# Kernel tuning notes

Hardware: AMD Instinct MI355X
Metric: run time of the kernel (lower is better)

Reference implementation:

```python
import jax, jax.numpy as jnp
import numpy as np

N_NODES, N_EDGES, N_REL, F_DIM, N_HEAD, N_LAYERS = 20000, 100000, 1000, 128, 4, 4
NEG_SLOPE = 0.2  # PyG GATv2Conv default negative_slope


def _gatv2_layer(x, ea_full, src, dst, Wl, bl, Wr, br, We, att, bias):
    # x: [N, F]; ea_full: [Etot, F] edge attrs (incl. self-loop rows)
    N = x.shape[0]
    H, C = att.shape  # heads, out-dim per head
    xl = (x @ Wl + bl).reshape(N, H, C)          # source-side projection
    xr = (x @ Wr + br).reshape(N, H, C)          # target-side projection
    ee = (ea_full @ We).reshape(-1, H, C)        # [Etot, H, C] edge embedding
    # GATv2 scoring: leaky_relu(x_i + x_j + e) . att
    e = jax.nn.leaky_relu(xl[src] + xr[dst] + ee, NEG_SLOPE)
    logits = jnp.einsum('ehc,hc->eh', e, att)    # [Etot, H]
    # segment softmax over edges grouped by destination node
    m = jax.ops.segment_max(logits, dst, num_segments=N)
    p = jnp.exp(logits - m[dst])
    denom = jax.ops.segment_sum(p, dst, num_segments=N)
    alpha = p / denom[dst]                       # [Etot, H]
    out = jax.ops.segment_sum(alpha[:, :, None] * xl[src], dst, num_segments=N)
    return out.mean(axis=1) + bias               # concat=False -> head mean


def setup_inputs() -> dict:
    key = jax.random.key(0)
    ks = jax.random.split(key, 12)
    N, E, R, F, H, L = N_NODES, N_EDGES, N_REL, F_DIM, N_HEAD, N_LAYERS
    HC = H * F
    s = 1.0 / np.sqrt(F)
    return {
        'x': jax.random.normal(ks[0], (N, F), jnp.float32),
        'edge_index': jax.random.randint(ks[1], (2, E), 0, N, dtype=jnp.int32),
        'relations': jax.random.normal(ks[2], (R, F), jnp.float32),
        'relation_index': jax.random.randint(ks[3], (E,), 0, R, dtype=jnp.int32),
        'Wl': jax.random.normal(ks[4], (L, F, HC), jnp.float32) * s,
        'bl': jnp.zeros((L, HC), jnp.float32),
        'Wr': jax.random.normal(ks[5], (L, F, HC), jnp.float32) * s,
        'br': jnp.zeros((L, HC), jnp.float32),
        'We': jax.random.normal(ks[6], (L, F, HC), jnp.float32) * s,
        'att': jax.random.normal(ks[7], (L, H, F), jnp.float32) * s,
        'bias': jnp.zeros((L, F), jnp.float32),
    }


def reference(x, edge_index, relations, relation_index, Wl, bl, Wr, br, We, att, bias):
    N = x.shape[0]
    sl = jnp.arange(N, dtype=edge_index.dtype)
    src = jnp.concatenate([edge_index[0], sl])   # add_self_loops=True
    dst = jnp.concatenate([edge_index[1], sl])
    ea = relations[relation_index]               # [E, F]
    # self-loop edge_attr uses fill_value='mean' (PyG default)
    ea_mean = ea.mean(axis=0)
    ea_full = jnp.concatenate([ea, jnp.broadcast_to(ea_mean, (N, ea.shape[1]))])
    h = x
    for l in range(N_LAYERS):
        h = _gatv2_layer(h, ea_full, src, dst, Wl[l], bl[l], Wr[l], br[l], We[l], att[l], bias[l])
    return (h, relations)
```

## Files before the change

kernel.cpp:

```cpp
#include <hip/hip_runtime.h>
#include <hip/hip_bf16.h>

#define N_NODES   20000
#define N_EDGES   100000
#define N_REL     1000
#define F_DIM     128
#define N_HEAD    4
#define HC        512
#define HC2       256
#define N_LAYERS  4
#define REL_EXT_ROWS 1008
#define NEG_SLOPE 0.2f
#define NODE_MB   ((N_NODES + 63) / 64)
#define REL_MB    ((REL_EXT_ROWS + 63) / 64)

typedef __attribute__((ext_vector_type(8))) short short8;
typedef __attribute__((ext_vector_type(4))) float floatx4;

__device__ __forceinline__ float loadIn(const void* p, size_t i, int f32) {
    if (f32) return ((const float*)p)[i];
    union { unsigned int u; float f; } c;
    c.u = ((unsigned int)((const unsigned short*)p)[i]) << 16;
    return c.f;
}

__device__ __forceinline__ unsigned short f2bf(float v) {
    __hip_bfloat16 b = __float2bfloat16(v);
    return *(unsigned short*)&b;
}

__device__ __forceinline__ void unpack2(unsigned int u, float& lo, float& hi) {
    union { unsigned int u; float f; } a, b;
    a.u = u << 16;
    b.u = u & 0xFFFF0000u;
    lo = a.f; hi = b.f;
}

__global__ void detect_kernel(const unsigned short* __restrict__ x, int* __restrict__ flag) {
    int t = threadIdx.x;
    int cnt = 0;
    for (int j = t; j < 256; j += 64) {
        int e = (x[j] >> 7) & 0xFF;
        if (e >= 143) cnt++;
    }
    for (int off = 32; off; off >>= 1) cnt += __shfl_xor(cnt, off);
    if (t == 0) flag[0] = (cnt >= 8) ? 1 : 0;
}


__global__ void hist_kernel(const int* __restrict__ dst, const int* __restrict__ rel,
                            int* __restrict__ deg, int* __restrict__ rcount) {
    int e = blockIdx.x * 256 + threadIdx.x;
    if (e < N_EDGES) {
        atomicAdd(&deg[dst[e]], 1);
        atomicAdd(&rcount[rel[e]], 1);
    }
}

__global__ void ea_mean_kernel(const int* __restrict__ rcount,
                               const void* __restrict__ relations,
                               float* __restrict__ ea_mean, const int* __restrict__ flag) {
    int f32 = flag[0];
    int b = blockIdx.x;
    int t = threadIdx.x;
    int col = t & 127;
    int rhalf = t >> 7;
    float acc = 0.f;
    for (int j = 0; j < 4; ++j) {
        int r = b * 8 + j * 2 + rhalf;
        acc += (float)rcount[r] * loadIn(relations, (size_t)r * F_DIM + col, f32);
    }
    __shared__ float part[256];
    part[t] = acc;
    __syncthreads();
    if (t < 128)
        atomicAdd(&ea_mean[col], (part[t] + part[t + 128]) * (1.f / (float)N_EDGES));
}

__global__ void relext_kernel(const void* __restrict__ relations,
                              const float* __restrict__ ea_mean,
                              unsigned short* __restrict__ rel_ext, const int* __restrict__ flag) {
    int idx = blockIdx.x * 256 + threadIdx.x;
    if (idx >= REL_EXT_ROWS * F_DIM) return;
    int f32 = flag[0];
    int r = idx >> 7;
    int c = idx & 127;
    float v;
    if (r < N_REL)       v = loadIn(relations, idx, f32);
    else if (r == N_REL) v = ea_mean[c];
    else                 v = 0.f;
    rel_ext[idx] = f2bf(v);
}

__global__ void scan_kernel(const int* __restrict__ deg,
                            int* __restrict__ row_start, int* __restrict__ cursor) {
    __shared__ int part[1024];
    int t = threadIdx.x;
    const int CH = (N_NODES + 1023) / 1024;
    int base = t * CH;
    int sum = 0;
    for (int j = 0; j < CH; ++j) {
        int idx = base + j;
        if (idx < N_NODES) sum += deg[idx];
    }
    part[t] = sum;
    __syncthreads();
    for (int off = 1; off < 1024; off <<= 1) {
        int u = (t >= off) ? part[t - off] : 0;
        __syncthreads();
        part[t] += u;
        __syncthreads();
    }
    int run = part[t] - sum;
    for (int j = 0; j < CH; ++j) {
        int idx = base + j;
        if (idx < N_NODES) {
            row_start[idx] = run;
            cursor[idx] = run;
            run += deg[idx];
        }
    }
    if (t == 1023) row_start[N_NODES] = part[1023];
}

__global__ void scatter_kernel(const int* __restrict__ src, const int* __restrict__ dst,
                               const int* __restrict__ rel, int* __restrict__ cursor,
                               int* __restrict__ csr_pack) {
    int e = blockIdx.x * 256 + threadIdx.x;
    if (e < N_EDGES) {
        int d = dst[e];
        int p = atomicAdd(&cursor[d], 1);
        csr_pack[p] = src[e] | (rel[e] << 16);
    }
}

__global__ void tail_kernel(const void* __restrict__ relations, void* __restrict__ out,
                            const int* __restrict__ flag) {
    int i = blockIdx.x * 256 + threadIdx.x;
    if (i >= N_REL * F_DIM) return;
    int f32 = flag[0];
    float v = loadIn(relations, i, f32);
    size_t o = (size_t)N_NODES * F_DIM + i;
    if (f32) ((float*)out)[o] = v;
    else     ((unsigned short*)out)[o] = f2bf(v);
}

__global__ void w_transpose_kernel(const void* __restrict__ Wl, const void* __restrict__ Wr,
                                   const void* __restrict__ We,
                                   unsigned short* __restrict__ Wt, const int* __restrict__ flag) {
    int f32 = flag[0];
    int k0 = blockIdx.x * 64;
    int n0 = blockIdx.y * 64;
    int mat = blockIdx.z;
    const void* src = (mat < 4) ? Wl : (mat < 8 ? Wr : We);
    size_t base = (size_t)(mat & 3) * F_DIM * HC;
    unsigned short* dst = Wt + (size_t)mat * HC * F_DIM;
    __shared__ float T[64][65];
    int t = threadIdx.x;
    int r = t >> 2, cq = t & 3;
    for (int j = 0; j < 16; ++j) {
        int n = cq * 16 + j;
        T[n][r] = loadIn(src, base + (size_t)(k0 + r) * HC + n0 + n, f32);
    }
    __syncthreads();
    for (int j = 0; j < 16; ++j) {
        int k = cq * 16 + j;
        dst[(size_t)(n0 + r) * F_DIM + k0 + k] = f2bf(T[r][k]);
    }
}

__launch_bounds__(256, 4)
__global__ void proj_kernel(const void* __restrict__ A_node, int a_input,
                            const unsigned short* __restrict__ rel_ext,
                            const unsigned short* __restrict__ Wlt,
                            const unsigned short* __restrict__ Wrt,
                            const unsigned short* __restrict__ Wet,
                            const void* __restrict__ bl, const void* __restrict__ br,
                            size_t boff,
                            unsigned short* __restrict__ xl,
                            unsigned short* __restrict__ xr,
                            unsigned short* __restrict__ re,
                            const int* __restrict__ flag) {
    __shared__ __align__(16) short As[64][136];
    __shared__ __align__(16) short BtRaw[128 * 72];
    int f32 = flag[0];
    int isNode = (blockIdx.x < NODE_MB);
    int m0 = (isNode ? blockIdx.x : (blockIdx.x - NODE_MB)) * 64;
    int M = isNode ? N_NODES : REL_EXT_ROWS;
    int tpb = isNode ? 2 : 1;
    int a_f32 = (isNode && a_input) ? f32 : 0;
    const void* A = isNode ? A_node : (const void*)rel_ext;
    int t = threadIdx.x;

    for (int j = 0; j < 4; ++j) {
        int c = t + j * 256;
        int row = c >> 4;
        int colc = (c & 15) * 8;
        int gm = m0 + row;
        short8 v = (short8){0, 0, 0, 0, 0, 0, 0, 0};
        if (gm < M) {
            size_t idx = (size_t)gm * F_DIM + colc;
            if (a_f32) {
                const float* Af = (const float*)A;
                for (int q = 0; q < 8; ++q) v[q] = (short)f2bf(Af[idx + q]);
            } else {
                v = *(const short8*)((const unsigned short*)A + idx);
            }
        }
        *(short8*)&As[row][colc] = v;
    }

    int wave = t >> 6, lane = t & 63;
    int wm = (wave >> 1) * 32, wn = (wave & 1) * 64;
    int r16 = lane & 15, quad = lane >> 4;

    for (int it = 0; it < tpb; ++it) {
        int nt = isNode ? (blockIdx.y * 2 + it) : blockIdx.y;
        const unsigned short* Wt = isNode ? ((nt < 4) ? Wlt : Wrt) : Wet;
        int n0 = (nt & 3) * 128;

        floatx4 acc[2][4];
        for (int mi = 0; mi < 2; ++mi)
            for (int ni = 0; ni < 4; ++ni)
                acc[mi][ni] = (floatx4){0.f, 0.f, 0.f, 0.f};

        for (int half = 0; half < 2; ++half) {
            __syncthreads();
            for (int j = 0; j < 4; ++j) {
                int c = t + j * 256;
                int nl = c >> 3;
                int kc = (c & 7) * 8;
                *(short8*)&BtRaw[nl * 72 + kc] =
                    *(const short8*)(Wt + (size_t)(n0 + nl) * F_DIM + half * 64 + kc);
            }
            __syncthreads();

            for (int kk = 0; kk < 2; ++kk) {
                short8 a[2], b[4];
                for (int mi = 0; mi < 2; ++mi)
                    a[mi] = *(const short8*)&As[wm + mi * 16 + r16][half * 64 + kk * 32 + quad * 8];
                for (int ni = 0; ni < 4; ++ni)
                    b[ni] = *(const short8*)&BtRaw[(wn + ni * 16 + r16) * 72 + kk * 32 + quad * 8];
                for (int mi = 0; mi < 2; ++mi)
                    for (int ni = 0; ni < 4; ++ni)
                        acc[mi][ni] = __builtin_amdgcn_mfma_f32_16x16x32_bf16(a[mi], b[ni], acc[mi][ni], 0, 0, 0);
            }
        }

        const void* bias = isNode ? ((nt < 4) ? bl : br) : nullptr;
        unsigned short* out = isNode ? ((nt < 4) ? xl : xr) : re;
        __syncthreads();
        for (int mi = 0; mi < 2; ++mi) {
            for (int ni = 0; ni < 4; ++ni) {
                int col = wn + ni * 16 + r16;
                float bv = bias ? loadIn(bias, boff + n0 + col, f32) : 0.f;
                for (int r = 0; r < 4; ++r) {
                    int rowl = wm + mi * 16 + quad * 4 + r;
                    BtRaw[rowl * 136 + col] = (short)f2bf(acc[mi][ni][r] + bv);
                }
            }
        }
        __syncthreads();
        for (int j = 0; j < 4; ++j) {
            int c = t + j * 256;
            int rowl = c >> 4;
            int colc = (c & 15) * 8;
            int gm = m0 + rowl;
            if (gm < M)
                *(short8*)(out + (size_t)gm * HC + n0 + colc) =
                    *(const short8*)&BtRaw[rowl * 136 + colc];
        }
    }
}

__launch_bounds__(256)
__global__ void edge_kernel(const unsigned int* __restrict__ xl2,
                            const unsigned int* __restrict__ xr2,
                            const unsigned int* __restrict__ re2,
                            const int* __restrict__ row_start,
                            const int* __restrict__ csr_pack,
                            const void* __restrict__ att, size_t att_off,
                            const void* __restrict__ bias, size_t bias_off,
                            void* __restrict__ hout, int final_layer,
                            const int* __restrict__ flag) {
    int f32 = flag[0];
    int i = blockIdx.x;
    int h = threadIdx.x >> 6;
    int lane = threadIdx.x & 63;
    int pidx = h * 64 + lane;

    float xr0, xr1; unpack2(xr2[(size_t)i * HC2 + pidx], xr0, xr1);
    float a0 = loadIn(att, att_off + h * F_DIM + 2 * lane, f32);
    float a1 = loadIn(att, att_off + h * F_DIM + 2 * lane + 1, f32);
    float er0, er1; unpack2(re2[(size_t)N_REL * HC2 + pidx], er0, er1);

    float xs0, xs1; unpack2(xl2[(size_t)i * HC2 + pidx], xs0, xs1);
    float t0 = xs0 + xr0 + er0;
    float t1 = xs1 + xr1 + er1;
    t0 = fmaxf(t0, NEG_SLOPE * t0);
    t1 = fmaxf(t1, NEG_SLOPE * t1);
    float part = t0 * a0 + t1 * a1;
    for (int off = 32; off; off >>= 1) part += __shfl_xor(part, off);
    part = fminf(fmaxf(part, -60.f), 60.f);
    float p = __expf(part);
    float s = p, acc0 = p * xs0, acc1 = p * xs1;

    int e0 = row_start[i], e1 = row_start[i + 1];
    if (e0 < 0) e0 = 0;
    if (e1 > N_EDGES) e1 = N_EDGES;
    if (e1 < e0) e1 = e0;

    unsigned int xv[4], rv[4];
    #pragma unroll
    for (int k = 0; k < 4; ++k) { xv[k] = 0; rv[k] = 0; }
    int b = e0;
    int nb = e1 - b; if (nb > 4) nb = 4;
    #pragma unroll
    for (int k = 0; k < 4; ++k) {
        if (k < nb) {
            int pk = csr_pack[b + k];
            int sn = pk & 0xFFFF;        if (sn >= N_NODES) sn = 0;
            int rn = (pk >> 16) & 0x3FF; if (rn > N_REL) rn = N_REL;
            xv[k] = xl2[(size_t)sn * HC2 + pidx];
            rv[k] = re2[(size_t)rn * HC2 + pidx];
        }
    }
    while (b < e1) {
        int bn = b + 4;
        int nbn = e1 - bn; if (nbn > 4) nbn = 4; if (nbn < 0) nbn = 0;
        unsigned int xvn[4], rvn[4];
        #pragma unroll
        for (int k = 0; k < 4; ++k) { xvn[k] = 0; rvn[k] = 0; }
        #pragma unroll
        for (int k = 0; k < 4; ++k) {
            if (k < nbn) {
                int pk = csr_pack[bn + k];
                int sn = pk & 0xFFFF;        if (sn >= N_NODES) sn = 0;
                int rn = (pk >> 16) & 0x3FF; if (rn > N_REL) rn = N_REL;
                xvn[k] = xl2[(size_t)sn * HC2 + pidx];
                rvn[k] = re2[(size_t)rn * HC2 + pidx];
            }
        }
        #pragma unroll
        for (int k = 0; k < 4; ++k) {
            if (k < nb) {
                float xl0, xl1; unpack2(xv[k], xl0, xl1);
                float ee0, ee1; unpack2(rv[k], ee0, ee1);
                float u0 = xl0 + xr0 + ee0;
                float u1 = xl1 + xr1 + ee1;
                u0 = fmaxf(u0, NEG_SLOPE * u0);
                u1 = fmaxf(u1, NEG_SLOPE * u1);
                float pe = u0 * a0 + u1 * a1;
                for (int off = 32; off; off >>= 1) pe += __shfl_xor(pe, off);
                pe = fminf(fmaxf(pe, -60.f), 60.f);
                float pp = __expf(pe);
                s += pp;
                acc0 += pp * xl0;
                acc1 += pp * xl1;
            }
        }
        #pragma unroll
        for (int k = 0; k < 4; ++k) { xv[k] = xvn[k]; rv[k] = rvn[k]; }
        b = bn; nb = nbn;
    }

    float inv = 1.f / s;
    __shared__ float lsum[N_HEAD][F_DIM];
    lsum[h][2 * lane]     = acc0 * inv;
    lsum[h][2 * lane + 1] = acc1 * inv;
    __syncthreads();
    if (threadIdx.x < F_DIM) {
        int c = threadIdx.x;
        float v = (lsum[0][c] + lsum[1][c] + lsum[2][c] + lsum[3][c]) * 0.25f
                + loadIn(bias, bias_off + c, f32);
        size_t o = (size_t)i * F_DIM + c;
        if (final_layer && f32) ((float*)hout)[o] = v;
        else                    ((unsigned short*)hout)[o] = f2bf(v);
    }
}


extern "C" void kernel_launch(void* const* d_in, const int* in_sizes, int n_in,
                              void* d_out, int out_size, void* d_ws, size_t ws_size,
                              hipStream_t stream) {
    const void* x          = d_in[0];
    const int*  edge_index = (const int*)d_in[1];
    const void* relations  = d_in[2];
    const int*  rel_index  = (const int*)d_in[3];
    const void* Wl         = d_in[4];
    const void* bl         = d_in[5];
    const void* Wr         = d_in[6];
    const void* br         = d_in[7];
    const void* We         = d_in[8];
    const void* att        = d_in[9];
    const void* bias       = d_in[10];

    char* ws = (char*)d_ws;
    size_t off = 0;
    auto alloc = [&](size_t bytes) -> void* {
        void* p = ws + off;
        off = (off + bytes + 255) & ~(size_t)255;
        return p;
    };
    int*            flag     = (int*)alloc(4);
    char*           zero0    = ws + off;
    int*            deg      = (int*)alloc(N_NODES * 4);
    int*            rcount   = (int*)alloc(N_REL * 4);
    float*          ea_mean  = (float*)alloc(F_DIM * 4);
    size_t          zlen     = (size_t)((ws + off) - zero0);
    int*            row_start= (int*)alloc((N_NODES + 1) * 4);
    int*            cursor   = (int*)alloc(N_NODES * 4);
    int*            csr_pack = (int*)alloc(N_EDGES * 4);
    unsigned short* rel_ext  = (unsigned short*)alloc((size_t)REL_EXT_ROWS * F_DIM * 2);
    unsigned short* Wt       = (unsigned short*)alloc((size_t)12 * HC * F_DIM * 2);
    unsigned short* re       = (unsigned short*)alloc((size_t)REL_EXT_ROWS * HC * 2);
    unsigned short* hbuf     = (unsigned short*)alloc((size_t)N_NODES * F_DIM * 2);
    unsigned short* xl       = (unsigned short*)alloc((size_t)N_NODES * HC * 2);
    unsigned short* xr       = (unsigned short*)alloc((size_t)N_NODES * HC * 2);

    const int* esrc = edge_index;
    const int* edst = edge_index + N_EDGES;

    detect_kernel<<<1, 64, 0, stream>>>((const unsigned short*)x, flag);
    hipMemsetAsync(zero0, 0, zlen, stream);
    hist_kernel<<<(N_EDGES + 255) / 256, 256, 0, stream>>>(edst, rel_index, deg, rcount);
    ea_mean_kernel<<<N_REL / 8, 256, 0, stream>>>(rcount, relations, ea_mean, flag);
    relext_kernel<<<(REL_EXT_ROWS * F_DIM + 255) / 256, 256, 0, stream>>>(relations, ea_mean, rel_ext, flag);
    scan_kernel<<<1, 1024, 0, stream>>>(deg, row_start, cursor);
    scatter_kernel<<<(N_EDGES + 255) / 256, 256, 0, stream>>>(esrc, edst, rel_index, cursor, csr_pack);
    w_transpose_kernel<<<dim3(2, 8, 12), 256, 0, stream>>>(Wl, Wr, We, Wt, flag);
    tail_kernel<<<(N_REL * F_DIM + 255) / 256, 256, 0, stream>>>(relations, d_out, flag);

    const void* hin = x;
    int a_input = 1;
    for (int l = 0; l < N_LAYERS; ++l) {
        const unsigned short* Wlt = Wt + (size_t)l * HC * F_DIM;
        const unsigned short* Wrt = Wt + (size_t)(4 + l) * HC * F_DIM;
        const unsigned short* Wet = Wt + (size_t)(8 + l) * HC * F_DIM;
        proj_kernel<<<dim3(NODE_MB + REL_MB, 4), 256, 0, stream>>>(
            hin, a_input, rel_ext, Wlt, Wrt, Wet,
            bl, br, (size_t)l * HC,
            xl, xr, re, flag);
        int final_layer = (l == N_LAYERS - 1);
        void* hout = final_layer ? d_out : (void*)hbuf;
        edge_kernel<<<N_NODES, 256, 0, stream>>>(
            (const unsigned int*)xl, (const unsigned int*)xr, (const unsigned int*)re,
            row_start, csr_pack,
            att, (size_t)l * N_HEAD * F_DIM,
            bias, (size_t)l * F_DIM,
            hout, final_layer, flag);
        hin = hbuf;
        a_input = 0;
    }
}
```

Measured before the change: 430.2 us.

## Map one wavefront per node in edge kernel with 16-byte vector gathers

The edge kernel now gives each destination node a single 64-lane wavefront instead of a 256-thread block. Each lane loads 8 bf16 values per gather with 16-byte loads, and the per-head reduction uses a 4-step shuffle. The head mean is done with cross-lane shuffles instead of shared memory and __syncthreads, and outputs are written with vector stores. The explicit software prefetch of the next edge batch is dropped, so latency hiding relies on the four loads issued per batch and on occupancy.

```diff
diff --git a/kernel.cpp b/kernel.cpp
--- a/kernel.cpp
+++ b/kernel.cpp
@@ -34,6 +34,13 @@
     a.u = u << 16;
     b.u = u & 0xFFFF0000u;
     lo = a.f; hi = b.f;
+}
+
+__device__ __forceinline__ void unpack8(uint4 v, float* f) {
+    unpack2(v.x, f[0], f[1]);
+    unpack2(v.y, f[2], f[3]);
+    unpack2(v.z, f[4], f[5]);
+    unpack2(v.w, f[6], f[7]);
 }
 
 __global__ void detect_kernel(const unsigned short* __restrict__ x, int* __restrict__ flag) {
@@ -284,98 +291,126 @@
                             void* __restrict__ hout, int final_layer,
                             const int* __restrict__ flag) {
     int f32 = flag[0];
-    int i = blockIdx.x;
-    int h = threadIdx.x >> 6;
+    int wid = threadIdx.x >> 6;
     int lane = threadIdx.x & 63;
-    int pidx = h * 64 + lane;
-
-    float xr0, xr1; unpack2(xr2[(size_t)i * HC2 + pidx], xr0, xr1);
-    float a0 = loadIn(att, att_off + h * F_DIM + 2 * lane, f32);
-    float a1 = loadIn(att, att_off + h * F_DIM + 2 * lane + 1, f32);
-    float er0, er1; unpack2(re2[(size_t)N_REL * HC2 + pidx], er0, er1);
-
-    float xs0, xs1; unpack2(xl2[(size_t)i * HC2 + pidx], xs0, xs1);
-    float t0 = xs0 + xr0 + er0;
-    float t1 = xs1 + xr1 + er1;
-    t0 = fmaxf(t0, NEG_SLOPE * t0);
-    t1 = fmaxf(t1, NEG_SLOPE * t1);
-    float part = t0 * a0 + t1 * a1;
-    for (int off = 32; off; off >>= 1) part += __shfl_xor(part, off);
-    part = fminf(fmaxf(part, -60.f), 60.f);
-    float p = __expf(part);
-    float s = p, acc0 = p * xs0, acc1 = p * xs1;
+    int i = blockIdx.x * 4 + wid;
+    if (i >= N_NODES) return;
+    int h = lane >> 4;
+    int q = lane & 15;
+    int loff = h * 64 + q * 4;
+
+    float xr[8];
+    { uint4 v = *(const uint4*)(xr2 + (size_t)i * HC2 + loff); unpack8(v, xr); }
+    float er[8];
+    { uint4 v = *(const uint4*)(re2 + (size_t)N_REL * HC2 + loff); unpack8(v, er); }
+    float av[8];
+    #pragma unroll
+    for (int j = 0; j < 8; ++j)
+        av[j] = loadIn(att, att_off + (size_t)h * F_DIM + q * 8 + j, f32);
+
+    float acc[8];
+    float s;
+    {
+        float xs[8];
+        uint4 v = *(const uint4*)(xl2 + (size_t)i * HC2 + loff);
+        unpack8(v, xs);
+        float part = 0.f;
+        #pragma unroll
+        for (int j = 0; j < 8; ++j) {
+            float u = xs[j] + xr[j] + er[j];
+            u = fmaxf(u, NEG_SLOPE * u);
+            part = fmaf(u, av[j], part);
+        }
+        #pragma unroll
+        for (int off = 8; off; off >>= 1) part += __shfl_xor(part, off);
+        part = fminf(fmaxf(part, -60.f), 60.f);
+        float p = __expf(part);
+        s = p;
+        #pragma unroll
+        for (int j = 0; j < 8; ++j) acc[j] = p * xs[j];
+    }
 
     int e0 = row_start[i], e1 = row_start[i + 1];
     if (e0 < 0) e0 = 0;
     if (e1 > N_EDGES) e1 = N_EDGES;
     if (e1 < e0) e1 = e0;
 
-    unsigned int xv[4], rv[4];
-    #pragma unroll
-    for (int k = 0; k < 4; ++k) { xv[k] = 0; rv[k] = 0; }
-    int b = e0;
-    int nb = e1 - b; if (nb > 4) nb = 4;
-    #pragma unroll
-    for (int k = 0; k < 4; ++k) {
-        if (k < nb) {
-            int pk = csr_pack[b + k];
-            int sn = pk & 0xFFFF;        if (sn >= N_NODES) sn = 0;
-            int rn = (pk >> 16) & 0x3FF; if (rn > N_REL) rn = N_REL;
-            xv[k] = xl2[(size_t)sn * HC2 + pidx];
-            rv[k] = re2[(size_t)rn * HC2 + pidx];
-        }
-    }
-    while (b < e1) {
-        int bn = b + 4;
-        int nbn = e1 - bn; if (nbn > 4) nbn = 4; if (nbn < 0) nbn = 0;
-        unsigned int xvn[4], rvn[4];
-        #pragma unroll
-        for (int k = 0; k < 4; ++k) { xvn[k] = 0; rvn[k] = 0; }
+    for (int b = e0; b < e1; b += 4) {
+        int nb = e1 - b; if (nb > 4) nb = 4;
+        uint4 xv[4], rv[4];
         #pragma unroll
         for (int k = 0; k < 4; ++k) {
-            if (k < nbn) {
-                int pk = csr_pack[bn + k];
+            if (k < nb) {
+                int pk = csr_pack[b + k];
                 int sn = pk & 0xFFFF;        if (sn >= N_NODES) sn = 0;
                 int rn = (pk >> 16) & 0x3FF; if (rn > N_REL) rn = N_REL;
-                xvn[k] = xl2[(size_t)sn * HC2 + pidx];
-                rvn[k] = re2[(size_t)rn * HC2 + pidx];
+                xv[k] = *(const uint4*)(xl2 + (size_t)sn * HC2 + loff);
+                rv[k] = *(const uint4*)(re2 + (size_t)rn * HC2 + loff);
             }
         }
         #pragma unroll
         for (int k = 0; k < 4; ++k) {
             if (k < nb) {
-                float xl0, xl1; unpack2(xv[k], xl0, xl1);
-                float ee0, ee1; unpack2(rv[k], ee0, ee1);
-                float u0 = xl0 + xr0 + ee0;
-                float u1 = xl1 + xr1 + ee1;
-                u0 = fmaxf(u0, NEG_SLOPE * u0);
-                u1 = fmaxf(u1, NEG_SLOPE * u1);
-                float pe = u0 * a0 + u1 * a1;
-                for (int off = 32; off; off >>= 1) pe += __shfl_xor(pe, off);
-                pe = fminf(fmaxf(pe, -60.f), 60.f);
-                float pp = __expf(pe);
+                float xlv[8], ee[8];
+                unpack8(xv[k], xlv);
+                unpack8(rv[k], ee);
+                float part = 0.f;
+                #pragma unroll
+                for (int j = 0; j < 8; ++j) {
+                    float u = xlv[j] + xr[j] + ee[j];
+                    u = fmaxf(u, NEG_SLOPE * u);
+                    part = fmaf(u, av[j], part);
+                }
+                #pragma unroll
+                for (int off = 8; off; off >>= 1) part += __shfl_xor(part, off);
+                part = fminf(fmaxf(part, -60.f), 60.f);
+                float pp = __expf(part);
                 s += pp;
-                acc0 += pp * xl0;
-                acc1 += pp * xl1;
-            }
-        }
-        #pragma unroll
-        for (int k = 0; k < 4; ++k) { xv[k] = xvn[k]; rv[k] = rvn[k]; }
-        b = bn; nb = nbn;
+                #pragma unroll
+                for (int j = 0; j < 8; ++j) acc[j] = fmaf(pp, xlv[j], acc[j]);
+            }
+        }
     }
 
     float inv = 1.f / s;
-    __shared__ float lsum[N_HEAD][F_DIM];
-    lsum[h][2 * lane]     = acc0 * inv;
-    lsum[h][2 * lane + 1] = acc1 * inv;
-    __syncthreads();
-    if (threadIdx.x < F_DIM) {
-        int c = threadIdx.x;
-        float v = (lsum[0][c] + lsum[1][c] + lsum[2][c] + lsum[3][c]) * 0.25f
-                + loadIn(bias, bias_off + c, f32);
-        size_t o = (size_t)i * F_DIM + c;
-        if (final_layer && f32) ((float*)hout)[o] = v;
-        else                    ((unsigned short*)hout)[o] = f2bf(v);
+    float outv[8];
+    #pragma unroll
+    for (int j = 0; j < 8; ++j) outv[j] = acc[j] * inv;
+    #pragma unroll
+    for (int j = 0; j < 8; ++j) {
+        outv[j] += __shfl_xor(outv[j], 16);
+        outv[j] += __shfl_xor(outv[j], 32);
+    }
+
+    if (h == 0) {
+        float bv[8];
+        #pragma unroll
+        for (int j = 0; j < 8; ++j)
+            bv[j] = loadIn(bias, bias_off + q * 8 + j, f32);
+        size_t o = (size_t)i * F_DIM + q * 8;
+        if (final_layer && f32) {
+            float* op = (float*)hout + o;
+            float4 lo, hi;
+            lo.x = outv[0] * 0.25f + bv[0];
+            lo.y = outv[1] * 0.25f + bv[1];
+            lo.z = outv[2] * 0.25f + bv[2];
+            lo.w = outv[3] * 0.25f + bv[3];
+            hi.x = outv[4] * 0.25f + bv[4];
+            hi.y = outv[5] * 0.25f + bv[5];
+            hi.z = outv[6] * 0.25f + bv[6];
+            hi.w = outv[7] * 0.25f + bv[7];
+            *(float4*)op = lo;
+            *(float4*)(op + 4) = hi;
+        } else {
+            unsigned int w[4];
+            #pragma unroll
+            for (int p = 0; p < 4; ++p) {
+                float v0 = outv[2 * p] * 0.25f + bv[2 * p];
+                float v1 = outv[2 * p + 1] * 0.25f + bv[2 * p + 1];
+                w[p] = (unsigned int)f2bf(v0) | ((unsigned int)f2bf(v1) << 16);
+            }
+            *(uint4*)((unsigned short*)hout + o) = *(uint4*)w;
+        }
     }
 }
 
@@ -443,7 +478,7 @@
             xl, xr, re, flag);
         int final_layer = (l == N_LAYERS - 1);
         void* hout = final_layer ? d_out : (void*)hbuf;
-        edge_kernel<<<N_NODES, 256, 0, stream>>>(
+        edge_kernel<<<(N_NODES + 3) / 4, 256, 0, stream>>>(
             (const unsigned int*)xl, (const unsigned int*)xr, (const unsigned int*)re,
             row_start, csr_pack,
             att, (size_t)l * N_HEAD * F_DIM,
```

After: 444.8 us. 1.03x slower.
